# Optimization experiments

Hardware: AMD Instinct MI355X
Metric: run time of the kernel (lower is better)

Reference implementation:

```python
import jax, jax.numpy as jnp
import numpy as np

B, S, D = 2, 2048, 1024
H = 16
DK = D // H
SCALE = 1.0 / np.sqrt(DK)

def setup_inputs() -> dict:
    key = jax.random.key(0)
    ks = jax.random.split(key, 11)
    std = 1.0 / np.sqrt(D)
    return {
        "query": jax.random.normal(ks[0], (B, S, D), jnp.float32),
        "key":   jax.random.normal(ks[1], (B, S, D), jnp.float32),
        "value": jax.random.normal(ks[2], (B, S, D), jnp.float32),
        "Wq": jax.random.normal(ks[3], (D, H * DK), jnp.float32) * std,
        "bq": jnp.zeros((H * DK,), jnp.float32),
        "Wk": jax.random.normal(ks[4], (D, H * DK), jnp.float32) * std,
        "bk": jnp.zeros((H * DK,), jnp.float32),
        "Wv": jax.random.normal(ks[5], (D, H * DK), jnp.float32) * std,
        "bv": jnp.zeros((H * DK,), jnp.float32),
        "Wo": jax.random.normal(ks[6], (D, D), jnp.float32) * std,
        "bo": jnp.zeros((D,), jnp.float32),
    }

def reference(query, key, value, Wq, bq, Wk, bk, Wv, bv, Wo, bo):
    b, s, _ = query.shape
    # projections -> [b, s, h, d_k]
    q = (query @ Wq + bq).reshape(b, s, H, DK)
    k = (key   @ Wk + bk).reshape(b, s, H, DK)
    v = (value @ Wv + bv).reshape(b, s, H, DK)
    # scores [b, i, j, h]
    scores = jnp.einsum('bihd,bjhd->bijh', q, k) * SCALE
    attn = jax.nn.softmax(scores, axis=2)  # softmax over key dim j
    # dropout rate 0.0 (eval mode) -> identity
    x = jnp.einsum('bijh,bjhd->bihd', attn, v).reshape(b, s, H * DK)
    return x @ Wo + bo
```

## Files before the change

### kernel.cpp

```cpp
#include <hip/hip_runtime.h>
#include <hip/hip_bf16.h>
#include <math.h>
#include <stdint.h>

constexpr int Bb = 2, Ss = 2048, Dd = 1024, Hh = 16;
constexpr int Mm = Bb * Ss;
constexpr int Nn = Dd;
constexpr int Kk = Dd;
constexpr float QSCALE = 0.125f * 1.44269504088896340736f;

typedef unsigned short ushort_t;
typedef __attribute__((ext_vector_type(8))) short bf16x8;
typedef __attribute__((ext_vector_type(4))) float f32x4;

#if __has_builtin(__builtin_amdgcn_exp2f)
#define EXP2F(x) __builtin_amdgcn_exp2f(x)
#else
#define EXP2F(x) exp2f(x)
#endif

__device__ __forceinline__ ushort_t f2bf(float f) {
  union { float f; unsigned u; } v; v.f = f;
  return (ushort_t)((v.u + 0x7fff + ((v.u >> 16) & 1)) >> 16);
}

__device__ __forceinline__ void load16_lds(const void* g, void* l) {
  __builtin_amdgcn_global_load_lds(
      (const __attribute__((address_space(1))) void*)(uintptr_t)g,
      (__attribute__((address_space(3))) void*)(uint32_t)(uintptr_t)l, 16, 0, 0);
}

__global__ __launch_bounds__(256) void prep(
    const float* __restrict__ q, const float* __restrict__ k,
    const float* __restrict__ v, ushort_t* __restrict__ qkvb,
    const float* __restrict__ Wq, const float* __restrict__ Wk,
    const float* __restrict__ Wv, const float* __restrict__ Wo,
    ushort_t* __restrict__ Wt) {
  const int bid = blockIdx.x;
  const int tid = threadIdx.x;
  if (bid < 12288) {
    const int z = bid >> 12, xi = bid & 4095;
    const float* src = (z == 0) ? q : (z == 1) ? k : v;
    ushort_t* dst = qkvb + (size_t)z * Mm * Kk;
    const size_t idx = ((size_t)xi * 256 + tid) * 4;
    const float4 val = *(const float4*)(src + idx);
    ushort4 o;
    o.x = f2bf(val.x); o.y = f2bf(val.y); o.z = f2bf(val.z); o.w = f2bf(val.w);
    *(ushort4*)(dst + idx) = o;
    return;
  }
  const int bid2 = bid - 12288;
  const int z = bid2 >> 8, rem = bid2 & 255;
  const float* W = (z == 0) ? Wq : (z == 1) ? Wk : (z == 2) ? Wv : Wo;
  ushort_t* out = Wt + (size_t)z * Kk * Nn;
  __shared__ float t[64][65];
  const int n0 = (rem & 15) * 64, k0 = (rem >> 4) * 64;
  const int lr = tid >> 4, lc = (tid & 15) * 4;
#pragma unroll
  for (int i = 0; i < 4; i++) {
    const int r = lr + i * 16;
    const float4 vv = *(const float4*)(W + (size_t)(k0 + r) * Nn + n0 + lc);
    t[r][lc] = vv.x; t[r][lc + 1] = vv.y; t[r][lc + 2] = vv.z; t[r][lc + 3] = vv.w;
  }
  __syncthreads();
  const int n = tid >> 2, kc = (tid & 3) * 16;
  ushort_t tmp[16];
#pragma unroll
  for (int j = 0; j < 16; j++) tmp[j] = f2bf(t[kc + j][n]);
  ushort_t* op = out + (size_t)(n0 + n) * Kk + k0 + kc;
  ((uint4*)op)[0] = ((uint4*)tmp)[0];
  ((uint4*)op)[1] = ((uint4*)tmp)[1];
}

__global__ __launch_bounds__(256) void transpose_v(
    const ushort_t* __restrict__ Vp, ushort_t* __restrict__ Vt) {
  __shared__ ushort_t t[64][68];
  const int tid = threadIdx.x;
  const int s0 = blockIdx.x * 64, h = blockIdx.y, b = blockIdx.z;
  const int lr = tid >> 4, lc = (tid & 15) * 4;
#pragma unroll
  for (int i = 0; i < 4; i++) {
    const int r = lr + i * 16;
    const ushort4 v =
        *(const ushort4*)(Vp + (size_t)(b * Ss + s0 + r) * Dd + h * 64 + lc);
    *(ushort4*)&t[r][lc] = v;
  }
  __syncthreads();
  const int d = tid >> 2, sc = (tid & 3) * 16;
  ushort_t tmp[16];
#pragma unroll
  for (int j = 0; j < 16; j++) tmp[j] = t[sc + j][d];
  ushort_t* op = Vt + ((size_t)b * Dd + h * 64 + d) * Ss + s0 + sc;
  ((uint4*)op)[0] = ((uint4*)tmp)[0];
  ((uint4*)op)[1] = ((uint4*)tmp)[1];
}

template <int BN, bool OUT_BF16>
__global__ __launch_bounds__(256) void gemm_mfma(
    const ushort_t* __restrict__ Abase, size_t a_stride,
    const ushort_t* __restrict__ Wbase, size_t w_stride,
    const float* __restrict__ bias0, const float* __restrict__ bias1,
    const float* __restrict__ bias2, void* __restrict__ Cbase, size_t c_stride,
    float scale_z0) {
  constexpr int BM = 128, BK = 32;
  constexpr int WM = (BN == 128) ? 64 : 32;
  constexpr int MT_ = WM / 16, NT_ = 4;
  __shared__ ushort_t As[BM * BK];
  __shared__ ushort_t Bs[BN * BK];
  const int tid = threadIdx.x, lane = tid & 63, wid = tid >> 6;
  const int z = blockIdx.z;
  const ushort_t* A = Abase + (size_t)z * a_stride;
  const ushort_t* Wt = Wbase + (size_t)z * w_stride;
  const float* bias = (z == 0) ? bias0 : (z == 1) ? bias1 : bias2;
  const float sc = (z == 0) ? scale_z0 : 1.0f;
  const int m0 = blockIdx.y * BM, n0 = blockIdx.x * BN;
  const int wm = (BN == 128) ? (wid >> 1) * 64 : wid * 32;
  const int wn = (BN == 128) ? (wid & 1) * 64 : 0;
  const int quad = lane >> 4, r16 = lane & 15;
  const int srow = lane >> 2;
  const int scol = (lane & 3) * 8;

  f32x4 acc[MT_][NT_];
#pragma unroll
  for (int m = 0; m < MT_; m++)
#pragma unroll
    for (int n = 0; n < NT_; n++) acc[m][n] = f32x4{0.f, 0.f, 0.f, 0.f};

  for (int k0 = 0; k0 < Kk; k0 += BK) {
    __syncthreads();
#pragma unroll
    for (int i = 0; i < BM / 64; i++) {
      const int I = wid * (BM / 64) + i;
      load16_lds(A + (size_t)(m0 + I * 16 + srow) * Kk + k0 + scol, As + I * 512);
    }
#pragma unroll
    for (int i = 0; i < BN / 64; i++) {
      const int I = wid * (BN / 64) + i;
      load16_lds(Wt + (size_t)(n0 + I * 16 + srow) * Kk + k0 + scol, Bs + I * 512);
    }
    __syncthreads();
    bf16x8 af[MT_], bfr[NT_];
#pragma unroll
    for (int m = 0; m < MT_; m++)
      af[m] = *(const bf16x8*)(As + (wm + m * 16 + r16) * BK + quad * 8);
#pragma unroll
    for (int n = 0; n < NT_; n++)
      bfr[n] = *(const bf16x8*)(Bs + (wn + n * 16 + r16) * BK + quad * 8);
#pragma unroll
    for (int m = 0; m < MT_; m++)
#pragma unroll
      for (int n = 0; n < NT_; n++)
        acc[m][n] =
            __builtin_amdgcn_mfma_f32_16x16x32_bf16(af[m], bfr[n], acc[m][n], 0, 0, 0);
  }

#pragma unroll
  for (int m = 0; m < MT_; m++) {
#pragma unroll
    for (int n = 0; n < NT_; n++) {
      const int gc = n0 + wn + n * 16 + r16;
      const float bv = bias[gc];
#pragma unroll
      for (int r = 0; r < 4; r++) {
        const int gr = m0 + wm + m * 16 + quad * 4 + r;
        const float v = (acc[m][n][r] + bv) * sc;
        if (OUT_BF16)
          ((ushort_t*)Cbase)[(size_t)z * c_stride + (size_t)gr * Nn + gc] = f2bf(v);
        else
          ((float*)Cbase)[(size_t)z * c_stride + (size_t)gr * Nn + gc] = v;
      }
    }
  }
}

__global__ __launch_bounds__(256, 3) void flash_mfma(
    const ushort_t* __restrict__ Qp, const ushort_t* __restrict__ Kp,
    const ushort_t* __restrict__ Vt, ushort_t* __restrict__ Xp) {
  __shared__ __align__(16) char smem[34816];
  ushort_t* KsU = (ushort_t*)smem;
  ushort_t* VtsU = KsU + 8192;
  float* red = (float*)smem;

  const int tid = threadIdx.x, lane = tid & 63, wid = tid >> 6;
  const int lid = blockIdx.x + (blockIdx.y << 5) + (blockIdx.z << 9);
  const int swzb = ((lid & 7) << 7) + (lid >> 3);
  const int qt = swzb & 31, h = (swzb >> 5) & 15, b = swzb >> 9;
  const int quad = lane >> 4, r16 = lane & 15;
  const int row8 = lane >> 3;
  const int colsw = ((lane & 7) ^ row8) * 8;
  const int swz = r16 & 7;

  const ushort_t* Qg = Qp + ((size_t)(b * Ss + qt * 64)) * Dd + h * 64;
  const ushort_t* Kg = Kp + ((size_t)b * Ss) * Dd + h * 64;
  const ushort_t* Vg = Vt + ((size_t)b * Dd + h * 64) * Ss;

  bf16x8 qf[2][4];
#pragma unroll
  for (int n = 0; n < 4; n++)
#pragma unroll
    for (int ks = 0; ks < 2; ks++)
      qf[ks][n] = *(const bf16x8*)(Qg + (size_t)(n * 16 + r16) * Dd + ks * 32 + quad * 8);

  const uint32_t kbase = (uint32_t)(wid * 16 + r16) * 64;
  const uint32_t ko0 = (uint32_t)((quad ^ swz) << 3);
  const uint32_t ko1 = (uint32_t)(((4 + quad) ^ swz) << 3);
  const int vG = wid * 2 + (quad >> 1);
  const uint32_t vcol = (uint32_t)(((vG ^ swz) << 3) + (quad & 1) * 4);

  f32x4 acc[4][4];
#pragma unroll
  for (int mt = 0; mt < 4; mt++)
#pragma unroll
    for (int n = 0; n < 4; n++) acc[mt][n] = f32x4{0.f, 0.f, 0.f, 0.f};
  float rsn[4] = {0.f, 0.f, 0.f, 0.f};

  constexpr int NP = Ss / 128;

  auto stageK = [&](int pr) {
#pragma unroll
    for (int s = 0; s < 2; s++) {
      const int t64 = pr * 2 + s;
#pragma unroll
      for (int i = 0; i < 2; i++) {
        const int I = wid * 2 + i;
        load16_lds(Kg + (size_t)(t64 * 64 + I * 8 + row8) * Dd + colsw,
                   KsU + s * 4096 + I * 512);
      }
    }
  };
  auto stageV = [&](int pr) {
#pragma unroll
    for (int s = 0; s < 2; s++) {
      const int t64 = pr * 2 + s;
#pragma unroll
      for (int i = 0; i < 2; i++) {
        const int I = wid * 2 + i;
        load16_lds(Vg + (size_t)(I * 8 + row8) * Ss + t64 * 64 + colsw,
                   VtsU + s * 4096 + I * 512);
      }
    }
  };

  stageK(0);
  stageV(0);
  asm volatile("s_waitcnt vmcnt(0)" ::: "memory");
  __syncthreads();

  const ushort_t* KcA = KsU;
  const ushort_t* KcB = KsU + 4096;
  const ushort_t* VcA = VtsU;
  const ushort_t* VcB = VtsU + 4096;

  for (int p = 0; p < NP; p++) {
    asm volatile("s_waitcnt vmcnt(4)" ::: "memory");

    const bf16x8 kfA0 = *(const bf16x8*)(KcA + kbase + ko0);
    const bf16x8 kfA1 = *(const bf16x8*)(KcA + kbase + ko1);
    const bf16x8 kfB0 = *(const bf16x8*)(KcB + kbase + ko0);
    const bf16x8 kfB1 = *(const bf16x8*)(KcB + kbase + ko1);

    f32x4 sacc[4];
#pragma unroll
    for (int n = 0; n < 4; n++) sacc[n] = f32x4{0.f, 0.f, 0.f, 0.f};
    __builtin_amdgcn_s_setprio(1);
#pragma unroll
    for (int n = 0; n < 4; n++)
      sacc[n] = __builtin_amdgcn_mfma_f32_16x16x32_bf16(kfA0, qf[0][n], sacc[n], 0, 0, 0);
#pragma unroll
    for (int n = 0; n < 4; n++)
      sacc[n] = __builtin_amdgcn_mfma_f32_16x16x32_bf16(kfA1, qf[1][n], sacc[n], 0, 0, 0);
    __builtin_amdgcn_s_setprio(0);

    uint2 pA[4];
#pragma unroll
    for (int n = 0; n < 4; n++) {
      const float p0 = EXP2F(sacc[n][0]), p1 = EXP2F(sacc[n][1]);
      const float p2 = EXP2F(sacc[n][2]), p3 = EXP2F(sacc[n][3]);
      rsn[n] += (p0 + p1) + (p2 + p3);
      union { __hip_bfloat162 hh; unsigned u; } lo, hi;
      lo.hh = __float22bfloat162_rn(make_float2(p0, p1));
      hi.hh = __float22bfloat162_rn(make_float2(p2, p3));
      pA[n] = make_uint2(lo.u, hi.u);
    }

#pragma unroll
    for (int n = 0; n < 4; n++) sacc[n] = f32x4{0.f, 0.f, 0.f, 0.f};
    __builtin_amdgcn_s_setprio(1);
#pragma unroll
    for (int n = 0; n < 4; n++)
      sacc[n] = __builtin_amdgcn_mfma_f32_16x16x32_bf16(kfB0, qf[0][n], sacc[n], 0, 0, 0);
#pragma unroll
    for (int n = 0; n < 4; n++)
      sacc[n] = __builtin_amdgcn_mfma_f32_16x16x32_bf16(kfB1, qf[1][n], sacc[n], 0, 0, 0);
    __builtin_amdgcn_s_setprio(0);

    stageK((p + 1) & (NP - 1));

    bf16x8 pf[4];
#pragma unroll
    for (int n = 0; n < 4; n++) {
      const float p0 = EXP2F(sacc[n][0]), p1 = EXP2F(sacc[n][1]);
      const float p2 = EXP2F(sacc[n][2]), p3 = EXP2F(sacc[n][3]);
      rsn[n] += (p0 + p1) + (p2 + p3);
      union { __hip_bfloat162 hh; unsigned u; } lo, hi;
      lo.hh = __float22bfloat162_rn(make_float2(p0, p1));
      hi.hh = __float22bfloat162_rn(make_float2(p2, p3));
      union { uint4 u; bf16x8 v; } pk;
      pk.u = make_uint4(pA[n].x, pA[n].y, lo.u, hi.u);
      pf[n] = pk.v;
    }

    asm volatile("s_waitcnt vmcnt(4)\n\ts_barrier" ::: "memory");

    __builtin_amdgcn_s_setprio(1);
#pragma unroll
    for (int mt = 0; mt < 4; mt++) {
      const uint2 vA = *(const uint2*)(VcA + (uint32_t)(mt * 16 + r16) * 64 + vcol);
      const uint2 vB = *(const uint2*)(VcB + (uint32_t)(mt * 16 + r16) * 64 + vcol);
      union { uint4 u; bf16x8 v; } vk;
      vk.u = make_uint4(vA.x, vA.y, vB.x, vB.y);
#pragma unroll
      for (int n = 0; n < 4; n++)
        acc[mt][n] = __builtin_amdgcn_mfma_f32_16x16x32_bf16(vk.v, pf[n], acc[mt][n], 0, 0, 0);
    }
    __builtin_amdgcn_s_setprio(0);

    asm volatile("s_barrier" ::: "memory");
    stageV((p + 1) & (NP - 1));
  }

  asm volatile("s_waitcnt vmcnt(0)" ::: "memory");

#pragma unroll
  for (int n = 0; n < 4; n++) {
    float r = rsn[n];
    r += __shfl_xor(r, 16, 64);
    r += __shfl_xor(r, 32, 64);
    rsn[n] = r;
  }

  __syncthreads();
  if (wid & 2) {
    float* p = red + (size_t)(wid & 1) * (64 * 68) + (size_t)lane * 68;
#pragma unroll
    for (int mt = 0; mt < 4; mt++)
#pragma unroll
      for (int n = 0; n < 4; n++)
        *(f32x4*)(p + (mt * 4 + n) * 4) = acc[mt][n];
    p[64] = rsn[0]; p[65] = rsn[1]; p[66] = rsn[2]; p[67] = rsn[3];
  }
  __syncthreads();
  if (!(wid & 2)) {
    const float* p = red + (size_t)wid * (64 * 68) + (size_t)lane * 68;
#pragma unroll
    for (int mt = 0; mt < 4; mt++)
#pragma unroll
      for (int n = 0; n < 4; n++)
        acc[mt][n] += *(const f32x4*)(p + (mt * 4 + n) * 4);
    rsn[0] += p[64]; rsn[1] += p[65]; rsn[2] += p[66]; rsn[3] += p[67];
  }
  __syncthreads();
  if (wid == 1) {
    float* p = red + (size_t)lane * 68;
#pragma unroll
    for (int mt = 0; mt < 4; mt++)
#pragma unroll
      for (int n = 0; n < 4; n++)
        *(f32x4*)(p + (mt * 4 + n) * 4) = acc[mt][n];
    p[64] = rsn[0]; p[65] = rsn[1]; p[66] = rsn[2]; p[67] = rsn[3];
  }
  __syncthreads();
  if (wid == 0) {
    const float* p = red + (size_t)lane * 68;
#pragma unroll
    for (int mt = 0; mt < 4; mt++)
#pragma unroll
      for (int n = 0; n < 4; n++)
        acc[mt][n] += *(const f32x4*)(p + (mt * 4 + n) * 4);
    rsn[0] += p[64]; rsn[1] += p[65]; rsn[2] += p[66]; rsn[3] += p[67];
    float inv[4];
#pragma unroll
    for (int n = 0; n < 4; n++) inv[n] = 1.0f / rsn[n];
#pragma unroll
    for (int mt = 0; mt < 4; mt++) {
#pragma unroll
      for (int n = 0; n < 4; n++) {
        ushort4 o;
        o.x = f2bf(acc[mt][n][0] * inv[n]);
        o.y = f2bf(acc[mt][n][1] * inv[n]);
        o.z = f2bf(acc[mt][n][2] * inv[n]);
        o.w = f2bf(acc[mt][n][3] * inv[n]);
        *(ushort4*)(Xp + (size_t)(b * Ss + qt * 64 + n * 16 + r16) * Dd +
                    h * 64 + mt * 16 + quad * 4) = o;
      }
    }
  }
}

extern "C" void kernel_launch(void* const* d_in, const int* in_sizes, int n_in,
                              void* d_out, int out_size, void* d_ws,
                              size_t ws_size, hipStream_t stream) {
  const float* q  = (const float*)d_in[0];
  const float* k  = (const float*)d_in[1];
  const float* v  = (const float*)d_in[2];
  const float* Wq = (const float*)d_in[3];
  const float* bq = (const float*)d_in[4];
  const float* Wk = (const float*)d_in[5];
  const float* bk = (const float*)d_in[6];
  const float* Wv = (const float*)d_in[7];
  const float* bv = (const float*)d_in[8];
  const float* Wo = (const float*)d_in[9];
  const float* bo = (const float*)d_in[10];

  ushort_t* ws = (ushort_t*)d_ws;
  const size_t MD = (size_t)Mm * Kk;
  const size_t KN = (size_t)Kk * Nn;
  ushort_t* qkvb = ws;
  ushort_t* Wt   = ws + 3 * MD;
  ushort_t* QKVp = Wt + 4 * KN;
  ushort_t* Vtp  = QKVp + 3 * MD;
  ushort_t* Xp   = qkvb;

  prep<<<dim3(13312), 256, 0, stream>>>(q, k, v, qkvb, Wq, Wk, Wv, Wo, Wt);
  gemm_mfma<128, true><<<dim3(Nn / 128, Mm / 128, 3), 256, 0, stream>>>(
      qkvb, MD, Wt, KN, bq, bk, bv, QKVp, MD, QSCALE);
  transpose_v<<<dim3(Ss / 64, Hh, Bb), 256, 0, stream>>>(QKVp + 2 * MD, Vtp);
  flash_mfma<<<dim3(Ss / 64, Hh, Bb), 256, 0, stream>>>(QKVp, QKVp + MD, Vtp, Xp);
  gemm_mfma<64, false><<<dim3(Nn / 64, Mm / 128, 1), 256, 0, stream>>>(
      Xp, 0, Wt + 3 * KN, 0, bo, bo, bo, d_out, 0, 1.0f);
}
```

Baseline: 232.0 us.

## Fuse V transpose into QKV GEMM epilogue and add XCD-aware block swizzle

```diff
diff --git a/kernel.cpp b/kernel.cpp
--- a/kernel.cpp
+++ b/kernel.cpp
@@ -72,36 +72,13 @@
   ((uint4*)op)[1] = ((uint4*)tmp)[1];
 }
 
-__global__ __launch_bounds__(256) void transpose_v(
-    const ushort_t* __restrict__ Vp, ushort_t* __restrict__ Vt) {
-  __shared__ ushort_t t[64][68];
-  const int tid = threadIdx.x;
-  const int s0 = blockIdx.x * 64, h = blockIdx.y, b = blockIdx.z;
-  const int lr = tid >> 4, lc = (tid & 15) * 4;
-#pragma unroll
-  for (int i = 0; i < 4; i++) {
-    const int r = lr + i * 16;
-    const ushort4 v =
-        *(const ushort4*)(Vp + (size_t)(b * Ss + s0 + r) * Dd + h * 64 + lc);
-    *(ushort4*)&t[r][lc] = v;
-  }
-  __syncthreads();
-  const int d = tid >> 2, sc = (tid & 3) * 16;
-  ushort_t tmp[16];
-#pragma unroll
-  for (int j = 0; j < 16; j++) tmp[j] = t[sc + j][d];
-  ushort_t* op = Vt + ((size_t)b * Dd + h * 64 + d) * Ss + s0 + sc;
-  ((uint4*)op)[0] = ((uint4*)tmp)[0];
-  ((uint4*)op)[1] = ((uint4*)tmp)[1];
-}
-
-template <int BN, bool OUT_BF16>
+template <int BN, bool OUT_BF16, bool VT_Z2>
 __global__ __launch_bounds__(256) void gemm_mfma(
     const ushort_t* __restrict__ Abase, size_t a_stride,
     const ushort_t* __restrict__ Wbase, size_t w_stride,
     const float* __restrict__ bias0, const float* __restrict__ bias1,
     const float* __restrict__ bias2, void* __restrict__ Cbase, size_t c_stride,
-    float scale_z0) {
+    float scale_z0, ushort_t* __restrict__ vt_out) {
   constexpr int BM = 128, BK = 32;
   constexpr int WM = (BN == 128) ? 64 : 32;
   constexpr int MT_ = WM / 16, NT_ = 4;
@@ -113,7 +90,11 @@
   const ushort_t* Wt = Wbase + (size_t)z * w_stride;
   const float* bias = (z == 0) ? bias0 : (z == 1) ? bias1 : bias2;
   const float sc = (z == 0) ? scale_z0 : 1.0f;
-  const int m0 = blockIdx.y * BM, n0 = blockIdx.x * BN;
+  const int nxy = gridDim.x * gridDim.y;
+  const int lid0 = blockIdx.x + gridDim.x * blockIdx.y;
+  const int cpx = nxy >> 3;
+  const int swb = (lid0 & 7) * cpx + (lid0 >> 3);
+  const int m0 = (swb / gridDim.x) * BM, n0 = (swb % gridDim.x) * BN;
   const int wm = (BN == 128) ? (wid >> 1) * 64 : wid * 32;
   const int wn = (BN == 128) ? (wid & 1) * 64 : 0;
   const int quad = lane >> 4, r16 = lane & 15;
@@ -152,6 +133,26 @@
       for (int n = 0; n < NT_; n++)
         acc[m][n] =
             __builtin_amdgcn_mfma_f32_16x16x32_bf16(af[m], bfr[n], acc[m][n], 0, 0, 0);
+  }
+
+  if (VT_Z2 && z == 2) {
+#pragma unroll
+    for (int m = 0; m < MT_; m++) {
+#pragma unroll
+      for (int n = 0; n < NT_; n++) {
+        const int gc = n0 + wn + n * 16 + r16;
+        const float bv = bias[gc];
+        const int gr0 = m0 + wm + m * 16 + quad * 4;
+        const int bb = gr0 >> 11, s0 = gr0 & 2047;
+        ushort4 o;
+        o.x = f2bf(acc[m][n][0] + bv);
+        o.y = f2bf(acc[m][n][1] + bv);
+        o.z = f2bf(acc[m][n][2] + bv);
+        o.w = f2bf(acc[m][n][3] + bv);
+        *(ushort4*)(vt_out + ((size_t)bb * Dd + gc) * Ss + s0) = o;
+      }
+    }
+    return;
   }
 
 #pragma unroll
@@ -422,10 +423,9 @@
   ushort_t* Xp   = qkvb;
 
   prep<<<dim3(13312), 256, 0, stream>>>(q, k, v, qkvb, Wq, Wk, Wv, Wo, Wt);
-  gemm_mfma<128, true><<<dim3(Nn / 128, Mm / 128, 3), 256, 0, stream>>>(
-      qkvb, MD, Wt, KN, bq, bk, bv, QKVp, MD, QSCALE);
-  transpose_v<<<dim3(Ss / 64, Hh, Bb), 256, 0, stream>>>(QKVp + 2 * MD, Vtp);
+  gemm_mfma<128, true, true><<<dim3(Nn / 128, Mm / 128, 3), 256, 0, stream>>>(
+      qkvb, MD, Wt, KN, bq, bk, bv, QKVp, MD, QSCALE, Vtp);
   flash_mfma<<<dim3(Ss / 64, Hh, Bb), 256, 0, stream>>>(QKVp, QKVp + MD, Vtp, Xp);
-  gemm_mfma<64, false><<<dim3(Nn / 64, Mm / 128, 1), 256, 0, stream>>>(
-      Xp, 0, Wt + 3 * KN, 0, bo, bo, bo, d_out, 0, 1.0f);
-}
+  gemm_mfma<64, false, false><<<dim3(Nn / 64, Mm / 128, 1), 256, 0, stream>>>(
+      Xp, 0, Wt + 3 * KN, 0, bo, bo, bo, d_out, 0, 1.0f, nullptr);
+}
```

New measurement: 234.7 us. Within noise of the previous version (+1.2%).

## Double-buffer GEMM LDS tiles with async prefetch, block swizzle, and MFMA priority

Applied to the files above, without the earlier changes.

```diff
diff --git a/kernel.cpp b/kernel.cpp
--- a/kernel.cpp
+++ b/kernel.cpp
@@ -105,15 +105,21 @@
   constexpr int BM = 128, BK = 32;
   constexpr int WM = (BN == 128) ? 64 : 32;
   constexpr int MT_ = WM / 16, NT_ = 4;
-  __shared__ ushort_t As[BM * BK];
-  __shared__ ushort_t Bs[BN * BK];
+  constexpr int NKT = Kk / BK;
+  constexpr int LA = BM / 64, LB = BN / 64;
+  __shared__ ushort_t As[2][BM * BK];
+  __shared__ ushort_t Bs[2][BN * BK];
   const int tid = threadIdx.x, lane = tid & 63, wid = tid >> 6;
   const int z = blockIdx.z;
   const ushort_t* A = Abase + (size_t)z * a_stride;
   const ushort_t* Wt = Wbase + (size_t)z * w_stride;
   const float* bias = (z == 0) ? bias0 : (z == 1) ? bias1 : bias2;
   const float sc = (z == 0) ? scale_z0 : 1.0f;
-  const int m0 = blockIdx.y * BM, n0 = blockIdx.x * BN;
+  const int nxy = gridDim.x * gridDim.y;
+  const int lid0 = blockIdx.x + gridDim.x * blockIdx.y;
+  const int cpx = nxy >> 3;
+  const int swb = (lid0 & 7) * cpx + (lid0 >> 3);
+  const int m0 = (swb / gridDim.x) * BM, n0 = (swb % gridDim.x) * BN;
   const int wm = (BN == 128) ? (wid >> 1) * 64 : wid * 32;
   const int wn = (BN == 128) ? (wid & 1) * 64 : 0;
   const int quad = lane >> 4, r16 = lane & 15;
@@ -126,32 +132,55 @@
 #pragma unroll
     for (int n = 0; n < NT_; n++) acc[m][n] = f32x4{0.f, 0.f, 0.f, 0.f};
 
-  for (int k0 = 0; k0 < Kk; k0 += BK) {
-    __syncthreads();
-#pragma unroll
-    for (int i = 0; i < BM / 64; i++) {
-      const int I = wid * (BM / 64) + i;
-      load16_lds(A + (size_t)(m0 + I * 16 + srow) * Kk + k0 + scol, As + I * 512);
-    }
-#pragma unroll
-    for (int i = 0; i < BN / 64; i++) {
-      const int I = wid * (BN / 64) + i;
-      load16_lds(Wt + (size_t)(n0 + I * 16 + srow) * Kk + k0 + scol, Bs + I * 512);
-    }
-    __syncthreads();
+  auto stage = [&](int kt, int bsel) {
+    const int k0 = kt * BK;
+#pragma unroll
+    for (int i = 0; i < LA; i++) {
+      const int I = wid * LA + i;
+      load16_lds(A + (size_t)(m0 + I * 16 + srow) * Kk + k0 + scol,
+                 &As[bsel][I * 512]);
+    }
+#pragma unroll
+    for (int i = 0; i < LB; i++) {
+      const int I = wid * LB + i;
+      load16_lds(Wt + (size_t)(n0 + I * 16 + srow) * Kk + k0 + scol,
+                 &Bs[bsel][I * 512]);
+    }
+  };
+
+  stage(0, 0);
+  asm volatile("s_waitcnt vmcnt(0)" ::: "memory");
+  __syncthreads();
+
+  for (int kt = 0; kt < NKT; kt++) {
+    const int cur = kt & 1;
+    if (kt + 1 < NKT) {
+      stage(kt + 1, cur ^ 1);
+      if constexpr (LA + LB == 4)
+        asm volatile("s_waitcnt vmcnt(4)\n\ts_barrier" ::: "memory");
+      else
+        asm volatile("s_waitcnt vmcnt(3)\n\ts_barrier" ::: "memory");
+    } else {
+      asm volatile("s_waitcnt vmcnt(0)\n\ts_barrier" ::: "memory");
+    }
+
     bf16x8 af[MT_], bfr[NT_];
 #pragma unroll
     for (int m = 0; m < MT_; m++)
-      af[m] = *(const bf16x8*)(As + (wm + m * 16 + r16) * BK + quad * 8);
+      af[m] = *(const bf16x8*)(&As[cur][(wm + m * 16 + r16) * BK + quad * 8]);
 #pragma unroll
     for (int n = 0; n < NT_; n++)
-      bfr[n] = *(const bf16x8*)(Bs + (wn + n * 16 + r16) * BK + quad * 8);
+      bfr[n] = *(const bf16x8*)(&Bs[cur][(wn + n * 16 + r16) * BK + quad * 8]);
+    __builtin_amdgcn_s_setprio(1);
 #pragma unroll
     for (int m = 0; m < MT_; m++)
 #pragma unroll
       for (int n = 0; n < NT_; n++)
         acc[m][n] =
             __builtin_amdgcn_mfma_f32_16x16x32_bf16(af[m], bfr[n], acc[m][n], 0, 0, 0);
+    __builtin_amdgcn_s_setprio(0);
+
+    asm volatile("s_barrier" ::: "memory");
   }
 
 #pragma unroll
```

New measurement: 226.8 us. 2.2% less time.
